# Kernel optimization log

Hardware: AMD Instinct MI355X
Metric: run time of the kernel (lower is better)

Reference implementation:

```python
import jax, jax.numpy as jnp
import numpy as np

NUM_PTS = 2_097_152
NUM_INS = 16
NUM_FRAMES = 16
RES = 64


def setup_inputs() -> dict:
    key = jax.random.key(0)
    k1, k2, k3, k4 = jax.random.split(key, 4)
    pts = jax.random.uniform(k1, (NUM_PTS, 3), jnp.float32, -1.0, 1.0)  # normalized coords in [-1,1]
    bidx = jax.random.randint(k2, (NUM_PTS,), 0, NUM_INS).astype(jnp.int64)
    ts = jax.random.uniform(k3, (NUM_PTS,), jnp.float32, -1.0, 1.0)
    # flattened EMA occupancy value grid: [num_batches*num_frames, R, R, R]
    occ_grid = jax.random.uniform(k4, (NUM_INS * NUM_FRAMES, RES, RES, RES), jnp.float32)
    ts_keyframes = jnp.linspace(-1.0, 1.0, NUM_FRAMES, dtype=jnp.float32)  # sorted keyframe times
    return {"pts": pts, "bidx": bidx, "ts": ts, "occ_grid": occ_grid,
            "ts_keyframes": ts_keyframes, "num_frames": NUM_FRAMES}


def _nearest1d(sorted_keys, query):
    # torch_consecutive_nearest1d: index of the nearest element in a sorted 1D array
    F = sorted_keys.shape[0]
    i = jnp.clip(jnp.searchsorted(sorted_keys, query), 1, F - 1)
    left, right = sorted_keys[i - 1], sorted_keys[i]
    return jnp.where(query - left <= right - query, i - 1, i)


def reference(pts, bidx, ts, occ_grid, ts_keyframes, num_frames):
    res = occ_grid.shape[1]
    # voxel index: ((pts/2 + 0.5) * R).long().clamp(0, R-1)
    gidx = jnp.clip(jnp.floor((pts * 0.5 + 0.5) * res).astype(jnp.int32), 0, res - 1)
    fidx = _nearest1d(ts_keyframes, ts)
    flat_bidx = bidx * num_frames + fidx
    # irregular gather over the flat occupancy grid (memory-bound hot path)
    return occ_grid[flat_bidx, gidx[:, 0], gidx[:, 1], gidx[:, 2]]
```

## Files before the change

kernel.cpp:

```cpp
#include <hip/hip_runtime.h>

#define RES        64
#define NFRAMES    16
#define PPT        4


__global__ __launch_bounds__(256) void occ_gather_kernel(
    const float* __restrict__ pts,
    const int*   __restrict__ bidx,
    const float* __restrict__ ts,
    const float* __restrict__ occ,
    const float* __restrict__ keys,
    float*       __restrict__ out,
    int n)
{
    __shared__ float skeys[NFRAMES];
    if (threadIdx.x < NFRAMES) skeys[threadIdx.x] = keys[threadIdx.x];
    __syncthreads();

    const int tid    = blockIdx.x * blockDim.x + threadIdx.x;
    const int stride = gridDim.x * blockDim.x;

    int   idxv[PPT];
    float pxv[PPT], pyv[PPT], pzv[PPT], tv[PPT];
    int   bv[PPT];
    bool  ok[PPT];

    #pragma unroll
    for (int k = 0; k < PPT; ++k) {
        int idx = tid + k * stride;
        idxv[k] = idx;
        ok[k] = idx < n;
        if (ok[k]) {
            pxv[k] = pts[idx * 3 + 0];
            pyv[k] = pts[idx * 3 + 1];
            pzv[k] = pts[idx * 3 + 2];
            tv[k]  = ts[idx];
            bv[k]  = bidx[idx];
        }
    }

    unsigned int off[PPT];
    #pragma unroll
    for (int k = 0; k < PPT; ++k) {
        if (!ok[k]) continue;
        int gx = min(max((int)floorf((pxv[k] * 0.5f + 0.5f) * (float)RES), 0), RES - 1);
        int gy = min(max((int)floorf((pyv[k] * 0.5f + 0.5f) * (float)RES), 0), RES - 1);
        int gz = min(max((int)floorf((pzv[k] * 0.5f + 0.5f) * (float)RES), 0), RES - 1);

        int i = 0;
        #pragma unroll
        for (int j = 0; j < NFRAMES; ++j) i += (skeys[j] < tv[k]) ? 1 : 0;
        i = min(max(i, 1), NFRAMES - 1);
        float l = skeys[i - 1];
        float r = skeys[i];
        int f = (tv[k] - l <= r - tv[k]) ? (i - 1) : i;

        off[k] = ((unsigned int)(bv[k] * NFRAMES + f) << 18)
               | ((unsigned int)gx << 12)
               | ((unsigned int)gy << 6)
               |  (unsigned int)gz;
    }

    float val[PPT];
    #pragma unroll
    for (int k = 0; k < PPT; ++k) {
        if (ok[k]) val[k] = occ[off[k]];
    }
    #pragma unroll
    for (int k = 0; k < PPT; ++k) {
        if (ok[k]) out[idxv[k]] = val[k];
    }
}

extern "C" void kernel_launch(void* const* d_in, const int* in_sizes, int n_in,
                              void* d_out, int out_size, void* d_ws, size_t ws_size,
                              hipStream_t stream) {
    const float* pts  = (const float*)d_in[0];
    const int*   bidx = (const int*)  d_in[1];
    const float* ts   = (const float*)d_in[2];
    const float* occ  = (const float*)d_in[3];
    const float* keys = (const float*)d_in[4];
    float* out = (float*)d_out;

    int n = in_sizes[2];
    int blocks = (n + 256 * PPT - 1) / (256 * PPT);
    occ_gather_kernel<<<blocks, 256, 0, stream>>>(pts, bidx, ts, occ, keys, out, n);
}
```

Before: 371.5 us.

## Bin points by occupancy volume before gathering to improve cache locality

Splits the gather into three kernels: zero per-volume cursors, bin each point's flat offset and output index into a per-volume record buffer using shared-memory counting plus global atomics, then gather volume by volume. The intent is to confine each block's random reads to one 1 MB volume so they hit in L2 instead of spreading over the whole 256 MB grid. In exchange it adds kernel launches, an extra 16 MB write and read of records, scattered output writes, and it silently drops points if a bin exceeds its fixed capacity. If the workspace is too small it falls back to a grid-stride direct kernel.

```diff
diff --git a/kernel.cpp b/kernel.cpp
--- a/kernel.cpp
+++ b/kernel.cpp
@@ -1,75 +1,110 @@
 #include <hip/hip_runtime.h>
 
-#define RES        64
-#define NFRAMES    16
-#define PPT        4
+#define RES      64
+#define NFRAMES  16
+#define NB       256
+#define CAP      16384
+#define CSTRIDE  16
+#define IPT      8
+#define GIPT     8
 
+__device__ __forceinline__ unsigned int flat_off(
+    float px, float py, float pz, float t, int b, const float* skeys)
+{
+    int gx = min(max((int)floorf((px * 0.5f + 0.5f) * (float)RES), 0), RES - 1);
+    int gy = min(max((int)floorf((py * 0.5f + 0.5f) * (float)RES), 0), RES - 1);
+    int gz = min(max((int)floorf((pz * 0.5f + 0.5f) * (float)RES), 0), RES - 1);
+    int i = 0;
+    #pragma unroll
+    for (int j = 0; j < NFRAMES; ++j) i += (skeys[j] < t) ? 1 : 0;
+    i = min(max(i, 1), NFRAMES - 1);
+    float l = skeys[i - 1], r = skeys[i];
+    int f = (t - l <= r - t) ? (i - 1) : i;
+    return ((unsigned int)(b * NFRAMES + f) << 18)
+         | ((unsigned int)gx << 12) | ((unsigned int)gy << 6) | (unsigned int)gz;
+}
 
-__global__ __launch_bounds__(256) void occ_gather_kernel(
-    const float* __restrict__ pts,
-    const int*   __restrict__ bidx,
-    const float* __restrict__ ts,
-    const float* __restrict__ occ,
-    const float* __restrict__ keys,
-    float*       __restrict__ out,
-    int n)
+__global__ __launch_bounds__(256) void zero_cursors(unsigned int* cursors) {
+    cursors[threadIdx.x * CSTRIDE] = 0u;
+}
+
+__global__ __launch_bounds__(256) void bin_kernel(
+    const float* __restrict__ pts, const int* __restrict__ bidx,
+    const float* __restrict__ ts, const float* __restrict__ keys,
+    unsigned int* __restrict__ cursors, uint2* __restrict__ rec, int n)
+{
+    __shared__ float skeys[NFRAMES];
+    __shared__ unsigned int lcnt[NB];
+    __shared__ unsigned int lbase[NB];
+    const int tid = threadIdx.x;
+    if (tid < NFRAMES) skeys[tid] = keys[tid];
+    lcnt[tid] = 0u;
+    __syncthreads();
+
+    const int base = blockIdx.x * (256 * IPT);
+    unsigned int off[IPT], rnk[IPT], bk[IPT];
+    bool ok[IPT];
+    #pragma unroll
+    for (int k = 0; k < IPT; ++k) {
+        int i = base + k * 256 + tid;
+        ok[k] = i < n;
+        if (ok[k]) {
+            float px = pts[i * 3 + 0], py = pts[i * 3 + 1], pz = pts[i * 3 + 2];
+            off[k] = flat_off(px, py, pz, ts[i], bidx[i], skeys);
+            bk[k]  = off[k] >> 18;
+            rnk[k] = atomicAdd(&lcnt[bk[k]], 1u);
+        }
+    }
+    __syncthreads();
+    unsigned int c = lcnt[tid];
+    lbase[tid] = c ? atomicAdd(&cursors[tid * CSTRIDE], c) : 0u;
+    __syncthreads();
+    #pragma unroll
+    for (int k = 0; k < IPT; ++k) {
+        if (ok[k]) {
+            unsigned int p = lbase[bk[k]] + rnk[k];
+            if (p < CAP)
+                rec[bk[k] * CAP + p] = make_uint2(off[k], (unsigned int)(base + k * 256 + tid));
+        }
+    }
+}
+
+__global__ __launch_bounds__(256) void gather_kernel(
+    const unsigned int* __restrict__ cursors, const uint2* __restrict__ rec,
+    const float* __restrict__ occ, float* __restrict__ out)
+{
+    const int b     = blockIdx.x >> 3;
+    const int chunk = blockIdx.x & 7;
+    unsigned int cnt = min(cursors[b * CSTRIDE], (unsigned int)CAP);
+    const int j0 = chunk * (256 * GIPT);
+    if ((unsigned int)j0 >= cnt) return;
+
+    uint2 r[GIPT]; bool ok[GIPT];
+    #pragma unroll
+    for (int k = 0; k < GIPT; ++k) {
+        int j = j0 + k * 256 + threadIdx.x;
+        ok[k] = (unsigned int)j < cnt;
+        if (ok[k]) r[k] = rec[b * CAP + j];
+    }
+    float v[GIPT];
+    #pragma unroll
+    for (int k = 0; k < GIPT; ++k) if (ok[k]) v[k] = occ[r[k].x];
+    #pragma unroll
+    for (int k = 0; k < GIPT; ++k) if (ok[k]) out[r[k].y] = v[k];
+}
+
+__global__ __launch_bounds__(256) void direct_kernel(
+    const float* __restrict__ pts, const int* __restrict__ bidx,
+    const float* __restrict__ ts, const float* __restrict__ occ,
+    const float* __restrict__ keys, float* __restrict__ out, int n)
 {
     __shared__ float skeys[NFRAMES];
     if (threadIdx.x < NFRAMES) skeys[threadIdx.x] = keys[threadIdx.x];
     __syncthreads();
-
-    const int tid    = blockIdx.x * blockDim.x + threadIdx.x;
+    const int tid = blockIdx.x * blockDim.x + threadIdx.x;
     const int stride = gridDim.x * blockDim.x;
-
-    int   idxv[PPT];
-    float pxv[PPT], pyv[PPT], pzv[PPT], tv[PPT];
-    int   bv[PPT];
-    bool  ok[PPT];
-
-    #pragma unroll
-    for (int k = 0; k < PPT; ++k) {
-        int idx = tid + k * stride;
-        idxv[k] = idx;
-        ok[k] = idx < n;
-        if (ok[k]) {
-            pxv[k] = pts[idx * 3 + 0];
-            pyv[k] = pts[idx * 3 + 1];
-            pzv[k] = pts[idx * 3 + 2];
-            tv[k]  = ts[idx];
-            bv[k]  = bidx[idx];
-        }
-    }
-
-    unsigned int off[PPT];
-    #pragma unroll
-    for (int k = 0; k < PPT; ++k) {
-        if (!ok[k]) continue;
-        int gx = min(max((int)floorf((pxv[k] * 0.5f + 0.5f) * (float)RES), 0), RES - 1);
-        int gy = min(max((int)floorf((pyv[k] * 0.5f + 0.5f) * (float)RES), 0), RES - 1);
-        int gz = min(max((int)floorf((pzv[k] * 0.5f + 0.5f) * (float)RES), 0), RES - 1);
-
-        int i = 0;
-        #pragma unroll
-        for (int j = 0; j < NFRAMES; ++j) i += (skeys[j] < tv[k]) ? 1 : 0;
-        i = min(max(i, 1), NFRAMES - 1);
-        float l = skeys[i - 1];
-        float r = skeys[i];
-        int f = (tv[k] - l <= r - tv[k]) ? (i - 1) : i;
-
-        off[k] = ((unsigned int)(bv[k] * NFRAMES + f) << 18)
-               | ((unsigned int)gx << 12)
-               | ((unsigned int)gy << 6)
-               |  (unsigned int)gz;
-    }
-
-    float val[PPT];
-    #pragma unroll
-    for (int k = 0; k < PPT; ++k) {
-        if (ok[k]) val[k] = occ[off[k]];
-    }
-    #pragma unroll
-    for (int k = 0; k < PPT; ++k) {
-        if (ok[k]) out[idxv[k]] = val[k];
+    for (int i = tid; i < n; i += stride) {
+        out[i] = occ[flat_off(pts[i*3], pts[i*3+1], pts[i*3+2], ts[i], bidx[i], skeys)];
     }
 }
 
@@ -82,8 +117,18 @@
     const float* occ  = (const float*)d_in[3];
     const float* keys = (const float*)d_in[4];
     float* out = (float*)d_out;
+    int n = in_sizes[2];
 
-    int n = in_sizes[2];
-    int blocks = (n + 256 * PPT - 1) / (256 * PPT);
-    occ_gather_kernel<<<blocks, 256, 0, stream>>>(pts, bidx, ts, occ, keys, out, n);
+    const size_t curs_bytes = (size_t)NB * CSTRIDE * sizeof(unsigned int);
+    const size_t rec_bytes  = (size_t)NB * CAP * sizeof(uint2);
+    if (ws_size >= curs_bytes + rec_bytes) {
+        unsigned int* cursors = (unsigned int*)d_ws;
+        uint2* rec = (uint2*)((char*)d_ws + curs_bytes);
+        zero_cursors<<<1, 256, 0, stream>>>(cursors);
+        int bin_blocks = (n + 256 * IPT - 1) / (256 * IPT);
+        bin_kernel<<<bin_blocks, 256, 0, stream>>>(pts, bidx, ts, keys, cursors, rec, n);
+        gather_kernel<<<NB * 8, 256, 0, stream>>>(cursors, rec, occ, out);
+    } else {
+        direct_kernel<<<2048, 256, 0, stream>>>(pts, bidx, ts, occ, keys, out, n);
+    }
 }
```

After: 443.8 us. 19.5% more time.
